# Kernel optimization log

Hardware: AMD Instinct MI355X
Metric: run time of the kernel (lower is better)

Reference implementation:

```python
import jax, jax.numpy as jnp
import numpy as np
from jax import lax

GRAVITY = 9.8
DT = 0.1
MAX_STEPS = 200


def _conv(x, w, b):
    # x: [N,C,H,W], w: [O,I,3,3] (PyTorch OIHW), padding=1 -> SAME
    y = lax.conv_general_dilated(x, w, window_strides=(1, 1), padding='SAME',
                                 dimension_numbers=('NCHW', 'OIHW', 'NCHW'))
    return y + b[None, :, None, None]


def _maxpool2(x):
    return lax.reduce_window(x, -jnp.inf, lax.max,
                             window_dimensions=(1, 1, 2, 2),
                             window_strides=(1, 1, 2, 2), padding='VALID')


def setup_inputs() -> dict:
    key = jax.random.key(0)
    ks = jax.random.split(key, 12)
    B = 256
    x = jax.random.normal(ks[0], (B, 12, 128, 128), dtype=jnp.float32)

    def he(k, shape, fan_in):
        return jax.random.normal(k, shape, dtype=jnp.float32) * np.float32(np.sqrt(2.0 / fan_in))

    w1 = he(ks[1], (32, 12, 3, 3), 12 * 9); b1 = jnp.zeros((32,), jnp.float32)
    w2 = he(ks[2], (64, 32, 3, 3), 32 * 9); b2 = jnp.zeros((64,), jnp.float32)
    w3 = he(ks[3], (64, 64, 3, 3), 64 * 9); b3 = jnp.zeros((64,), jnp.float32)
    w4 = he(ks[4], (64, 64, 3, 3), 64 * 9); b4 = jnp.zeros((64,), jnp.float32)
    wl1 = he(ks[5], (128, 64 * 8 * 8), 64 * 8 * 8); bl1 = jnp.zeros((128,), jnp.float32)
    wl2 = he(ks[6], (4, 128), 128); bl2 = jnp.zeros((4,), jnp.float32)
    return {'x': x, 'w1': w1, 'b1': b1, 'w2': w2, 'b2': b2, 'w3': w3, 'b3': b3,
            'w4': w4, 'b4': b4, 'wl1': wl1, 'bl1': bl1, 'wl2': wl2, 'bl2': bl2}


def _forward(x, w1, b1, w2, b2, w3, b3, w4, b4, wl1, bl1, wl2, bl2):
    h = _maxpool2(jax.nn.relu(_conv(x, w1, b1)))   # [B,32,64,64]
    h = _maxpool2(jax.nn.relu(_conv(h, w2, b2)))   # [B,64,32,32]
    h = _maxpool2(jax.nn.relu(_conv(h, w3, b3)))   # [B,64,16,16]
    h = _maxpool2(jax.nn.relu(_conv(h, w4, b4)))   # [B,64,8,8]
    h = h.reshape(h.shape[0], -1)                  # [B,4096]
    h = jax.nn.relu(h @ wl1.T + bl1)               # [B,128]
    state = h @ wl2.T + bl2                        # [B,4]

    px, py, vx, vy = state[:, 0], state[:, 1], state[:, 2], state[:, 3]

    def step(carry, _):
        cx, cy, cvy = carry
        nvy = cvy - GRAVITY * DT
        nx = cx + vx * DT
        ny = jnp.maximum(cy + nvy * DT, 0.0)
        return (nx, ny, nvy), None

    (fx, _, _), _ = lax.scan(step, (px, py, vy), None, length=MAX_STEPS)
    return fx


def reference(x, w1, b1, w2, b2, w3, b3, w4, b4, wl1, bl1, wl2, bl2):
    return _forward(x, w1, b1, w2, b2, w3, b3, w4, b4, wl1, bl1, wl2, bl2)
```

## Files before the change

kernel.cpp:

```cpp
#include <hip/hip_runtime.h>


typedef _Float16 f16;
typedef _Float16 f16x8 __attribute__((ext_vector_type(8)));
typedef _Float16 f16x4 __attribute__((ext_vector_type(4)));
typedef float f32x4 __attribute__((ext_vector_type(4)));
typedef float f32x16 __attribute__((ext_vector_type(16)));

__global__ __launch_bounds__(512)
void pack_weights(const float* __restrict__ w1, const float* __restrict__ w2,
                  const float* __restrict__ w3, const float* __restrict__ w4,
                  f16* __restrict__ apack) {
  int idx = blockIdx.x * 512 + threadIdx.x;
  int frag = idx >> 9;
  int e = idx & 511;
  int lane = e >> 3, j = e & 7;
  float v = 0.f;
  if (frag < 9) {
    int kh = frag / 3, kw = frag % 3;
    int oc = lane & 31;
    int ic = (lane >> 5) * 8 + j;
    if (ic < 12) v = w1[((oc * 12 + ic) * 3 + kh) * 3 + kw];
  } else if (frag < 45) {
    int f = frag - 9;
    int sh = f >> 2, og = f & 3;
    int kh = sh / 3, kw = sh % 3;
    int row16 = lane & 15, kg = lane >> 4;
    int oc = og * 16 + row16;
    int ic = kg * 8 + j;
    v = w2[((oc * 32 + ic) * 3 + kh) * 3 + kw];
  } else {
    const float* w = (frag < 117) ? w3 : w4;
    int f = frag - ((frag < 117) ? 45 : 117);
    int sk = f >> 2, og = f & 3;
    int sh = sk >> 1, ks = sk & 1;
    int kh = sh / 3, kw = sh % 3;
    int row16 = lane & 15, kg = lane >> 4;
    int oc = og * 16 + row16;
    int ic = ks * 32 + kg * 8 + j;
    v = w[((oc * 64 + ic) * 3 + kh) * 3 + kw];
  }
  apack[idx] = (f16)v;
}

__global__ __launch_bounds__(512, 4)
void conv1_mfma(const float* __restrict__ x, const f16* __restrict__ apack,
                const float* __restrict__ bias, f16* __restrict__ hout) {
  constexpr int W = 128, H = 128;
  constexpr int SR = 6, PADB = 48, ROWB = 130 * PADB;
  constexpr int TPB = 8;
  __shared__ char smem[2][SR * ROWB];
  const int tid = threadIdx.x;
  const int n = blockIdx.y;

  if (tid < 72) {
    int b = tid / 36, rem = tid % 36;
    int slot = rem / 6, r = rem % 6;
    int px = (r >= 3) ? 129 : 0;
    int ch = r % 3;
    *(float4*)(smem[b] + slot * ROWB + px * PADB + ch * 16) =
        make_float4(0.f, 0.f, 0.f, 0.f);
  }

  const int g = tid >> 4;
  const int l16 = tid & 15;
  const int Q = l16 >> 2, q = l16 & 3;
  float4 a[SR];

  auto load_tile = [&](int t) {
    const int r0 = (blockIdx.x * TPB + t) * 4;
#pragma unroll
    for (int sr = 0; sr < SR; ++sr) {
      const int ri = r0 + sr - 1;
      a[sr] = make_float4(0.f, 0.f, 0.f, 0.f);
      if (l16 < 12 && ri >= 0 && ri < H)
        a[sr] = *(const float4*)(x + ((size_t)(n * 12 + l16) * H + ri) * W + g * 4);
    }
  };
  auto write_tile = [&](char* buf) {
#pragma unroll
    for (int sr = 0; sr < SR; ++sr) {
      float4 t1, t2;
      {
        float sx = __shfl_xor(a[sr].x, 1), sy = __shfl_xor(a[sr].y, 1);
        float sz = __shfl_xor(a[sr].z, 1), sw = __shfl_xor(a[sr].w, 1);
        bool odd = q & 1;
        t1.x = odd ? sy : a[sr].x;  t1.y = odd ? a[sr].y : sx;
        t1.z = odd ? sw : a[sr].z;  t1.w = odd ? a[sr].w : sz;
      }
      {
        float sx = __shfl_xor(t1.x, 2), sy = __shfl_xor(t1.y, 2);
        float sz = __shfl_xor(t1.z, 2), sw = __shfl_xor(t1.w, 2);
        bool hi2 = q & 2;
        t2.x = hi2 ? sz : t1.x;  t2.y = hi2 ? sw : t1.y;
        t2.z = hi2 ? t1.z : sx;  t2.w = hi2 ? t1.w : sy;
      }
      f16x4 h = { (f16)t2.x, (f16)t2.y, (f16)t2.z, (f16)t2.w };
      *(f16x4*)(buf + sr * ROWB + (g * 4 + q + 1) * PADB + Q * 8) = h;
    }
  };

  const int wv = tid >> 6, l = tid & 63;
  const int rp = wv >> 2;
  const int pxb = (wv & 3) * 32;
  const int rl0 = rp * 2;
  const int ln = l & 31;
  const int hi = l >> 5;

  f16x8 A[9];
#pragma unroll
  for (int ks = 0; ks < 9; ++ks)
    A[ks] = *(const f16x8*)(apack + ((ks << 9) + (l << 3)));

  auto compute = [&](const char* buf, int tg) {
    f32x16 acc0 = (f32x16)0.f, acc1 = (f32x16)0.f;
#pragma unroll
    for (int ks = 0; ks < 9; ++ks) {
      const int kh = ks / 3, kw = ks % 3;
      const char* base = buf + (pxb + ln + kw) * PADB + hi * 16;
      f16x8 B0 = *(const f16x8*)(base + (rl0 + kh) * ROWB);
      acc0 = __builtin_amdgcn_mfma_f32_32x32x16_f16(A[ks], B0, acc0, 0, 0, 0);
      f16x8 B1 = *(const f16x8*)(base + (rl0 + 1 + kh) * ROWB);
      acc1 = __builtin_amdgcn_mfma_f32_32x32x16_f16(A[ks], B1, acc1, 0, 0, 0);
    }
    const int pr = tg * 2 + rp;
#pragma unroll
    for (int gg = 0; gg < 4; ++gg) {
      float v[4];
#pragma unroll
      for (int c = 0; c < 4; ++c) {
        float m = fmaxf(acc0[gg * 4 + c], acc1[gg * 4 + c]);
        v[c] = fmaxf(m, __shfl_xor(m, 1));
      }
      if ((l & 1) == 0) {
        const int pw = (pxb + ln) >> 1;
        const int oc0 = gg * 8 + hi * 4;
        f16x4 pk;
#pragma unroll
        for (int c = 0; c < 4; ++c)
          pk[c] = (f16)fmaxf(v[c] + bias[oc0 + c], 0.f);
        *(f16x4*)(hout + (((size_t)(n * 64 + pr) * 64 + pw) * 32 + oc0)) = pk;
      }
    }
  };

  load_tile(0);
  write_tile(smem[0]);
  __syncthreads();

  for (int t = 0; t < TPB; ++t) {
    if (t + 1 < TPB) load_tile(t + 1);
    compute(smem[t & 1], blockIdx.x * TPB + t);
    __syncthreads();
    if (t + 1 < TPB) {
      write_tile(smem[(t + 1) & 1]);
      __syncthreads();
    }
  }
}

template<int C, int W, int H, int BR, int KS, int PADB, int PGn, bool NCHW_OUT>
__global__ __launch_bounds__(256)
void conv_shift(const f16* __restrict__ hin, const f16* __restrict__ apack,
                const float* __restrict__ bias, void* __restrict__ hout) {
  constexpr int SR = BR + 2;
  constexpr int ROWB = (W + 2) * PADB;
  __shared__ char smem[SR * ROWB];
  const int tid = threadIdx.x;
  const int n = blockIdx.y;
  const int r0 = blockIdx.x * BR;
  constexpr int CPC = C / 8;
  constexpr int TOTC = SR * (W + 2) * CPC;
  constexpr int NITER = (TOTC + 255) / 256;
  {
    float4 stg[NITER];
#pragma unroll
    for (int it = 0; it < NITER; ++it) {
      const int t = tid + it * 256;
      float4 v = make_float4(0.f, 0.f, 0.f, 0.f);
      if (t < TOTC) {
        int sr = t / ((W + 2) * CPC);
        int rem = t - sr * ((W + 2) * CPC);
        int px = rem / CPC;
        int kc = rem - px * CPC;
        int ri = r0 + sr - 1;
        int gx = px - 1;
        if (ri >= 0 && ri < H && gx >= 0 && gx < W)
          v = *(const float4*)(hin + (((size_t)(n * H + ri) * W + gx) * C + kc * 8));
      }
      stg[it] = v;
    }
#pragma unroll
    for (int it = 0; it < NITER; ++it) {
      const int t = tid + it * 256;
      if (t < TOTC) {
        int sr = t / ((W + 2) * CPC);
        int rem = t - sr * ((W + 2) * CPC);
        int px = rem / CPC;
        int kc = rem - px * CPC;
        *(float4*)(smem + sr * ROWB + px * PADB + kc * 16) = stg[it];
      }
    }
  }
  __syncthreads();

  const int wv = tid >> 6, l = tid & 63;
  constexpr int WPP = W / (16 * PGn);
  const int rp = wv / WPP;
  const int pxb = (wv % WPP) * 16 * PGn;
  const int rl0 = rp * 2;
  const int lp = l & 15, kg = l >> 4;
  const int px0 = pxb + lp;

  f32x4 acc[2][PGn][4];
#pragma unroll
  for (int a = 0; a < 2; ++a)
#pragma unroll
    for (int b = 0; b < PGn; ++b)
#pragma unroll
      for (int c = 0; c < 4; ++c)
        acc[a][b][c] = (f32x4){0.f, 0.f, 0.f, 0.f};

#pragma unroll
  for (int sh = 0; sh < 9; ++sh) {
    const int kh = sh / 3, kw = sh % 3;
    f16x8 A[KS][4];
#pragma unroll
    for (int ks = 0; ks < KS; ++ks)
#pragma unroll
      for (int og = 0; og < 4; ++og)
        A[ks][og] = *(const f16x8*)(apack + ((((sh * KS + ks) * 4 + og) << 9) + (l << 3)));
#pragma unroll
    for (int rowi = 0; rowi < 2; ++rowi) {
      const char* base = smem + (rl0 + rowi + kh) * ROWB;
#pragma unroll
      for (int pg = 0; pg < PGn; ++pg) {
#pragma unroll
        for (int ks = 0; ks < KS; ++ks) {
          f16x8 B = *(const f16x8*)(base + (px0 + pg * 16 + kw) * PADB + ks * 64 + kg * 16);
#pragma unroll
          for (int og = 0; og < 4; ++og)
            acc[rowi][pg][og] =
                __builtin_amdgcn_mfma_f32_16x16x32_f16(A[ks][og], B, acc[rowi][pg][og], 0, 0, 0);
        }
      }
    }
  }
  constexpr int PH = H / 2, PW = W / 2;
  const int pr = blockIdx.x * (BR / 2) + rp;
#pragma unroll
  for (int pg = 0; pg < PGn; ++pg) {
#pragma unroll
    for (int og = 0; og < 4; ++og) {
      float v[4];
#pragma unroll
      for (int c = 0; c < 4; ++c) {
        float m = fmaxf(acc[0][pg][og][c], acc[1][pg][og][c]);
        v[c] = fmaxf(m, __shfl_xor(m, 1));
      }
      if ((l & 1) == 0) {
        const int pw = (pxb + pg * 16 + lp) >> 1;
        const int oc0 = og * 16 + kg * 4;
        if constexpr (NCHW_OUT) {
          float* o = (float*)hout;
#pragma unroll
          for (int c = 0; c < 4; ++c)
            o[(((size_t)n * 64 + oc0 + c) * PH + pr) * PW + pw] =
                fmaxf(v[c] + bias[oc0 + c], 0.f);
        } else {
          f16x4 pk;
#pragma unroll
          for (int c = 0; c < 4; ++c)
            pk[c] = (f16)fmaxf(v[c] + bias[oc0 + c], 0.f);
          *(f16x4*)((f16*)hout + (((size_t)(n * PH + pr) * PW + pw) * 64 + oc0)) = pk;
        }
      }
    }
  }
}

__global__ __launch_bounds__(1024)
void fc_head(const float* __restrict__ h4, const float* __restrict__ wl1,
             const float* __restrict__ bl1, const float* __restrict__ wl2,
             const float* __restrict__ bl2, float* __restrict__ out) {
  __shared__ float rows[2][4096];
  __shared__ float red[8 * 128 * 2];
  __shared__ float red2[2 * 128];
  const int tid = threadIdx.x;
  const int b0 = blockIdx.x * 2;
  {
    const float4* src = (const float4*)(h4 + (size_t)b0 * 4096);
    float4* dst = (float4*)rows;
    for (int t = tid; t < 2048; t += 1024) dst[t] = src[t];
  }
  __syncthreads();

  const int nn = tid & 127;
  const int ks = tid >> 7;
  const float4* wp = (const float4*)(wl1 + (size_t)nn * 4096 + ks * 512);
  const float4* x0 = (const float4*)(&rows[0][ks * 512]);
  const float4* x1 = (const float4*)(&rows[1][ks * 512]);
  float s0 = 0.f, s1 = 0.f;
#pragma unroll 8
  for (int i = 0; i < 128; ++i) {
    float4 w = wp[i], a = x0[i], b = x1[i];
    s0 = fmaf(w.x, a.x, fmaf(w.y, a.y, fmaf(w.z, a.z, fmaf(w.w, a.w, s0))));
    s1 = fmaf(w.x, b.x, fmaf(w.y, b.y, fmaf(w.z, b.z, fmaf(w.w, b.w, s1))));
  }
  red[(ks * 128 + nn) * 2 + 0] = s0;
  red[(ks * 128 + nn) * 2 + 1] = s1;
  __syncthreads();

  if (tid < 256) {
    const int r = tid >> 7, n2 = tid & 127;
    float h = bl1[n2];
#pragma unroll
    for (int k = 0; k < 8; ++k) h += red[(k * 128 + n2) * 2 + r];
    h = fmaxf(h, 0.f);
    red2[r * 128 + n2] = h * (wl2[n2] + 20.0f * wl2[256 + n2]);
  }
  __syncthreads();
#pragma unroll
  for (int s = 64; s > 0; s >>= 1) {
    if (tid < 2 * s) {
      int r = tid / s, i = tid - r * s;
      red2[r * 128 + i] += red2[r * 128 + i + s];
    }
    __syncthreads();
  }
  if (tid < 2) out[b0 + tid] = red2[tid * 128] + bl2[0] + 20.0f * bl2[2];
}

extern "C" void kernel_launch(void* const* d_in, const int* in_sizes, int n_in,
                              void* d_out, int out_size, void* d_ws, size_t ws_size,
                              hipStream_t stream) {
  const float* x   = (const float*)d_in[0];
  const float* w1  = (const float*)d_in[1];
  const float* b1  = (const float*)d_in[2];
  const float* w2  = (const float*)d_in[3];
  const float* b2  = (const float*)d_in[4];
  const float* w3  = (const float*)d_in[5];
  const float* b3  = (const float*)d_in[6];
  const float* w4  = (const float*)d_in[7];
  const float* b4  = (const float*)d_in[8];
  const float* wl1 = (const float*)d_in[9];
  const float* bl1 = (const float*)d_in[10];
  const float* wl2 = (const float*)d_in[11];
  const float* bl2 = (const float*)d_in[12];
  float* out = (float*)d_out;
  char* ws = (char*)d_ws;

  f16* apack = (f16*)ws;
  f16* h1 = (f16*)(ws + (1u << 20));
  f16* h2 = (f16*)(ws + 68157440u);
  f16* h3 = (f16*)(ws + 101711872u);
  float* h4 = (float*)(ws + 110100480u);

  pack_weights<<<189, 512, 0, stream>>>(w1, w2, w3, w4, apack);
  conv1_mfma<<<dim3(4, 256), 512, 0, stream>>>(x, apack, b1, h1);
  conv_shift<32, 64, 64, 4, 1, 80, 2, false><<<dim3(16, 256), 256, 0, stream>>>(
      h1, apack + 9 * 512, b2, (void*)h2);
  conv_shift<64, 32, 32, 8, 2, 144, 2, false><<<dim3(4, 256), 256, 0, stream>>>(
      h2, apack + 45 * 512, b3, (void*)h3);
  conv_shift<64, 16, 16, 8, 2, 144, 1, true><<<dim3(2, 256), 256, 0, stream>>>(
      h3, apack + 117 * 512, b4, (void*)h4);
  fc_head<<<128, 1024, 0, stream>>>(h4, wl1, bl1, wl2, bl2, out);
}
```

Before: 246.3 us.

## Use rolling 6-row ring buffer in conv1 to reuse halo rows

Replaces the double-buffered 6-row shared-memory tiles in conv1 with a single 6-slot circular buffer. Each iteration now loads and transposes only 4 new input rows and keeps the 2 halo rows from the previous tile, which cuts global loads and shuffle/convert work by about a third. It also halves shared memory per block and drops the min-blocks hint from launch_bounds. The cost is modular slot indexing in the inner MFMA loop and a less explicit occupancy target.

```diff
diff --git a/kernel.cpp b/kernel.cpp
--- a/kernel.cpp
+++ b/kernel.cpp
@@ -43,61 +43,53 @@
   apack[idx] = (f16)v;
 }
 
-__global__ __launch_bounds__(512, 4)
+__global__ __launch_bounds__(512)
 void conv1_mfma(const float* __restrict__ x, const f16* __restrict__ apack,
                 const float* __restrict__ bias, f16* __restrict__ hout) {
   constexpr int W = 128, H = 128;
-  constexpr int SR = 6, PADB = 48, ROWB = 130 * PADB;
+  constexpr int PADB = 48, ROWB = 130 * PADB;
   constexpr int TPB = 8;
-  __shared__ char smem[2][SR * ROWB];
+  __shared__ char smem[6 * ROWB];
   const int tid = threadIdx.x;
   const int n = blockIdx.y;
-
-  if (tid < 72) {
-    int b = tid / 36, rem = tid % 36;
-    int slot = rem / 6, r = rem % 6;
+  const int R0 = blockIdx.x * (TPB * 4);
+
+  if (tid < 36) {
+    int slot = tid / 6, r = tid % 6;
     int px = (r >= 3) ? 129 : 0;
     int ch = r % 3;
-    *(float4*)(smem[b] + slot * ROWB + px * PADB + ch * 16) =
+    *(float4*)(smem + slot * ROWB + px * PADB + ch * 16) =
         make_float4(0.f, 0.f, 0.f, 0.f);
   }
 
   const int g = tid >> 4;
   const int l16 = tid & 15;
   const int Q = l16 >> 2, q = l16 & 3;
-  float4 a[SR];
-
-  auto load_tile = [&](int t) {
-    const int r0 = (blockIdx.x * TPB + t) * 4;
-#pragma unroll
-    for (int sr = 0; sr < SR; ++sr) {
-      const int ri = r0 + sr - 1;
-      a[sr] = make_float4(0.f, 0.f, 0.f, 0.f);
-      if (l16 < 12 && ri >= 0 && ri < H)
-        a[sr] = *(const float4*)(x + ((size_t)(n * 12 + l16) * H + ri) * W + g * 4);
-    }
+
+  auto load_row = [&](int ri) -> float4 {
+    float4 v = make_float4(0.f, 0.f, 0.f, 0.f);
+    if (l16 < 12 && ri >= 0 && ri < H)
+      v = *(const float4*)(x + ((size_t)(n * 12 + l16) * H + ri) * W + g * 4);
+    return v;
   };
-  auto write_tile = [&](char* buf) {
-#pragma unroll
-    for (int sr = 0; sr < SR; ++sr) {
-      float4 t1, t2;
-      {
-        float sx = __shfl_xor(a[sr].x, 1), sy = __shfl_xor(a[sr].y, 1);
-        float sz = __shfl_xor(a[sr].z, 1), sw = __shfl_xor(a[sr].w, 1);
-        bool odd = q & 1;
-        t1.x = odd ? sy : a[sr].x;  t1.y = odd ? a[sr].y : sx;
-        t1.z = odd ? sw : a[sr].z;  t1.w = odd ? a[sr].w : sz;
-      }
-      {
-        float sx = __shfl_xor(t1.x, 2), sy = __shfl_xor(t1.y, 2);
-        float sz = __shfl_xor(t1.z, 2), sw = __shfl_xor(t1.w, 2);
-        bool hi2 = q & 2;
-        t2.x = hi2 ? sz : t1.x;  t2.y = hi2 ? sw : t1.y;
-        t2.z = hi2 ? t1.z : sx;  t2.w = hi2 ? t1.w : sy;
-      }
-      f16x4 h = { (f16)t2.x, (f16)t2.y, (f16)t2.z, (f16)t2.w };
-      *(f16x4*)(buf + sr * ROWB + (g * 4 + q + 1) * PADB + Q * 8) = h;
-    }
+  auto xpose_write = [&](float4 av, int slot) {
+    float4 t1, t2;
+    {
+      float sx = __shfl_xor(av.x, 1), sy = __shfl_xor(av.y, 1);
+      float sz = __shfl_xor(av.z, 1), sw = __shfl_xor(av.w, 1);
+      bool odd = q & 1;
+      t1.x = odd ? sy : av.x;  t1.y = odd ? av.y : sx;
+      t1.z = odd ? sw : av.z;  t1.w = odd ? av.w : sz;
+    }
+    {
+      float sx = __shfl_xor(t1.x, 2), sy = __shfl_xor(t1.y, 2);
+      float sz = __shfl_xor(t1.z, 2), sw = __shfl_xor(t1.w, 2);
+      bool hi2 = q & 2;
+      t2.x = hi2 ? sz : t1.x;  t2.y = hi2 ? sw : t1.y;
+      t2.z = hi2 ? t1.z : sx;  t2.w = hi2 ? t1.w : sy;
+    }
+    f16x4 h = { (f16)t2.x, (f16)t2.y, (f16)t2.z, (f16)t2.w };
+    *(f16x4*)(smem + slot * ROWB + (g * 4 + q + 1) * PADB + Q * 8) = h;
   };
 
   const int wv = tid >> 6, l = tid & 63;
@@ -112,50 +104,62 @@
   for (int ks = 0; ks < 9; ++ks)
     A[ks] = *(const f16x8*)(apack + ((ks << 9) + (l << 3)));
 
-  auto compute = [&](const char* buf, int tg) {
+  float4 a[6];
+#pragma unroll
+  for (int i = 0; i < 6; ++i) a[i] = load_row(R0 - 1 + i);
+#pragma unroll
+  for (int i = 0; i < 6; ++i) xpose_write(a[i], i);
+  __syncthreads();
+
+  int s0 = 0;
+  for (int t = 0; t < TPB; ++t) {
+    if (t + 1 < TPB) {
+#pragma unroll
+      for (int i = 0; i < 4; ++i) a[i] = load_row(R0 + 4 * t + 5 + i);
+    }
     f32x16 acc0 = (f32x16)0.f, acc1 = (f32x16)0.f;
 #pragma unroll
     for (int ks = 0; ks < 9; ++ks) {
       const int kh = ks / 3, kw = ks % 3;
-      const char* base = buf + (pxb + ln + kw) * PADB + hi * 16;
-      f16x8 B0 = *(const f16x8*)(base + (rl0 + kh) * ROWB);
+      int sl0 = s0 + rl0 + kh;     if (sl0 >= 6) sl0 -= 6;
+      int sl1 = s0 + rl0 + 1 + kh; if (sl1 >= 6) sl1 -= 6;
+      const char* bcol = smem + (pxb + ln + kw) * PADB + hi * 16;
+      f16x8 B0 = *(const f16x8*)(bcol + sl0 * ROWB);
       acc0 = __builtin_amdgcn_mfma_f32_32x32x16_f16(A[ks], B0, acc0, 0, 0, 0);
-      f16x8 B1 = *(const f16x8*)(base + (rl0 + 1 + kh) * ROWB);
+      f16x8 B1 = *(const f16x8*)(bcol + sl1 * ROWB);
       acc1 = __builtin_amdgcn_mfma_f32_32x32x16_f16(A[ks], B1, acc1, 0, 0, 0);
     }
-    const int pr = tg * 2 + rp;
-#pragma unroll
-    for (int gg = 0; gg < 4; ++gg) {
-      float v[4];
-#pragma unroll
-      for (int c = 0; c < 4; ++c) {
-        float m = fmaxf(acc0[gg * 4 + c], acc1[gg * 4 + c]);
-        v[c] = fmaxf(m, __shfl_xor(m, 1));
-      }
-      if ((l & 1) == 0) {
-        const int pw = (pxb + ln) >> 1;
-        const int oc0 = gg * 8 + hi * 4;
-        f16x4 pk;
-#pragma unroll
-        for (int c = 0; c < 4; ++c)
-          pk[c] = (f16)fmaxf(v[c] + bias[oc0 + c], 0.f);
-        *(f16x4*)(hout + (((size_t)(n * 64 + pr) * 64 + pw) * 32 + oc0)) = pk;
-      }
-    }
-  };
-
-  load_tile(0);
-  write_tile(smem[0]);
-  __syncthreads();
-
-  for (int t = 0; t < TPB; ++t) {
-    if (t + 1 < TPB) load_tile(t + 1);
-    compute(smem[t & 1], blockIdx.x * TPB + t);
+    {
+      const int pr = (R0 >> 1) + 2 * t + rp;
+#pragma unroll
+      for (int gg = 0; gg < 4; ++gg) {
+        float v[4];
+#pragma unroll
+        for (int c = 0; c < 4; ++c) {
+          float m = fmaxf(acc0[gg * 4 + c], acc1[gg * 4 + c]);
+          v[c] = fmaxf(m, __shfl_xor(m, 1));
+        }
+        if ((l & 1) == 0) {
+          const int pw = (pxb + ln) >> 1;
+          const int oc0 = gg * 8 + hi * 4;
+          f16x4 pk;
+#pragma unroll
+          for (int c = 0; c < 4; ++c)
+            pk[c] = (f16)fmaxf(v[c] + bias[oc0 + c], 0.f);
+          *(f16x4*)(hout + (((size_t)(n * 64 + pr) * 64 + pw) * 32 + oc0)) = pk;
+        }
+      }
+    }
     __syncthreads();
     if (t + 1 < TPB) {
-      write_tile(smem[(t + 1) & 1]);
+#pragma unroll
+      for (int i = 0; i < 4; ++i) {
+        int sl = s0 + i; if (sl >= 6) sl -= 6;
+        xpose_write(a[i], sl);
+      }
       __syncthreads();
     }
+    s0 += 4; if (s0 >= 6) s0 -= 6;
   }
 }
 
```

After: 227.4 us. 1.08x faster.
